# Optimization experiments

Measured on AMD Instinct MI355X. Metric: run time of the kernel, lower is better.

Reference implementation:

```python
import jax, jax.numpy as jnp
import numpy as np

N = 100000      # nodes
E = 1600000     # edges (avg degree 16)
IN_DIM = 128
H = 4           # num_heads
D = 16          # out_feats per head
EF = 32         # edge_feats
T = 8           # num_etypes
NEG_SLOPE = 0.2


def setup_inputs() -> dict:
    key = jax.random.key(0)
    ks = jax.random.split(key, 10)
    x = jax.random.normal(ks[0], (N, IN_DIM), dtype=jnp.float32)
    src = jax.random.randint(ks[1], (E,), 0, N)
    dst = jax.random.randint(ks[2], (E,), 0, N)
    etype = jax.random.randint(ks[3], (E,), 0, T)
    # learned params (xavier-ish scale)
    fc_W = jax.random.normal(ks[4], (IN_DIM, H * D), dtype=jnp.float32) * (2.0 / (IN_DIM + H * D)) ** 0.5
    fc_e_W = jax.random.normal(ks[5], (EF, H * EF), dtype=jnp.float32) * (2.0 / (EF + H * EF)) ** 0.5
    edge_emb = jax.random.normal(ks[6], (T, EF), dtype=jnp.float32)
    attn_l = jax.random.normal(ks[7], (H, D), dtype=jnp.float32) * (2.0 / (H * D)) ** 0.5
    attn_r = jax.random.normal(ks[8], (H, D), dtype=jnp.float32) * (2.0 / (H * D)) ** 0.5
    attn_e = jax.random.normal(ks[9], (H, EF), dtype=jnp.float32) * (2.0 / (H * EF)) ** 0.5
    return {"x": x, "src": src, "dst": dst, "etype": etype,
            "fc_W": fc_W, "fc_e_W": fc_e_W, "edge_emb": edge_emb,
            "attn_l": attn_l, "attn_r": attn_r, "attn_e": attn_e}


def reference(x, src, dst, etype, fc_W, fc_e_W, edge_emb, attn_l, attn_r, attn_e):
    n = x.shape[0]
    # node projection: [N, H, D]
    feat = (x @ fc_W).reshape(n, H, D)
    el = jnp.einsum('nhd,hd->nh', feat, attn_l)   # [N, H]
    er = jnp.einsum('nhd,hd->nh', feat, attn_r)   # [N, H]
    # per-etype edge scalar: edge_emb @ fc_e -> [T, H, EF] -> [T, H]
    ef = (edge_emb @ fc_e_W).reshape(T, H, EF)
    ee = jnp.einsum('the,he->th', ef, attn_e)
    # per-edge attention logits, leaky relu  [E, H]
    s = jax.nn.leaky_relu(el[src] + er[dst] + ee[etype], NEG_SLOPE)
    # edge_softmax over incoming edges of each dst (homogeneous graph)
    smax = jax.ops.segment_max(s, dst, num_segments=n)
    p = jnp.exp(s - smax[dst])
    denom = jax.ops.segment_sum(p, dst, num_segments=n)
    a = p / denom[dst]                             # [E, H]
    # gather-mul-scatter aggregation: sum_e a_e * feat[src_e]
    msg = feat[src] * a[:, :, None]                # [E, H, D]
    rst = jax.ops.segment_sum(msg, dst, num_segments=n)  # [N, H, D]
    return rst
```

## Files before the change

kernel.cpp:

```cpp
#include <hip/hip_runtime.h>

#define NH 4
#define HD 64
#define IN_DIM 128
#define NEG_SLOPE 0.2f
#define BN 64
#define NBMAX 1664
#define SLAB 2048
#define CHUNK 4096
#define EPT (CHUNK/512)
#define SBUFSZ 2048
#define NGEMM 256

typedef short bf8 __attribute__((ext_vector_type(8)));
typedef float f4  __attribute__((ext_vector_type(4)));

__device__ inline unsigned short f2bf(float f) {
  unsigned u = __float_as_uint(f);
  u += 0x7FFFu + ((u >> 16) & 1u);
  return (unsigned short)(u >> 16);
}

__global__ __launch_bounds__(512) void k_combo(
    const float* __restrict__ x, const float* __restrict__ fcW,
    const float* __restrict__ attn_l, const float* __restrict__ attn_r,
    unsigned short* __restrict__ featb, float4* __restrict__ el4, float4* __restrict__ er4,
    const int* __restrict__ src, const int* __restrict__ dst, const int* __restrict__ et,
    int* __restrict__ cntg, unsigned* __restrict__ ebuf,
    const float* __restrict__ edge_emb, const float* __restrict__ fc_e_W,
    const float* __restrict__ attn_e, float* __restrict__ ee,
    int n, int ne, int nb, int ngemm, int nchunks)
{
  __shared__ union {
    struct {
      int scnt[NBMAX];
      unsigned short sbase[NBMAX];
      unsigned short goff[NBMAX];
      unsigned sbuf[CHUNK];
      int wsm[8], wbs[8];
    } m;
    unsigned short wt[HD][IN_DIM + 8];
    float sef[8][128];
  } sm;

  const int t = threadIdx.x;
  const int lane = t & 63, wv = t >> 6;

  if (blockIdx.x < ngemm) {
    for (int idx = t; idx < IN_DIM * HD; idx += 512) {
      int k = idx >> 6, j = idx & 63;
      sm.wt[j][k] = f2bf(fcW[idx]);
    }
    __syncthreads();

    const int lr = lane & 15;
    const int lg = lane >> 4;
    float al[NH], ar[NH];
#pragma unroll
    for (int h = 0; h < NH; ++h) { al[h] = attn_l[h * 16 + lr]; ar[h] = attn_r[h * 16 + lr]; }

    const int ntp = (n + 127) >> 7;
    for (int tp = blockIdx.x; tp < ntp; tp += ngemm) {
      const int rowbase = tp * 128 + wv * 16;
      int arow = rowbase + lr;
      if (arow >= n) arow = n - 1;
      const float* xp = x + (size_t)arow * IN_DIM + lg * 8;

      f4 acc[4] = {};
#pragma unroll
      for (int kc = 0; kc < 4; ++kc) {
        float4 a0 = *(const float4*)(xp + kc * 32);
        float4 a1 = *(const float4*)(xp + kc * 32 + 4);
        bf8 af;
        af[0] = (short)f2bf(a0.x); af[1] = (short)f2bf(a0.y);
        af[2] = (short)f2bf(a0.z); af[3] = (short)f2bf(a0.w);
        af[4] = (short)f2bf(a1.x); af[5] = (short)f2bf(a1.y);
        af[6] = (short)f2bf(a1.z); af[7] = (short)f2bf(a1.w);
#pragma unroll
        for (int nt = 0; nt < 4; ++nt) {
          bf8 bfr = *(const bf8*)&sm.wt[nt * 16 + lr][kc * 32 + lg * 8];
          acc[nt] = __builtin_amdgcn_mfma_f32_16x16x32_bf16(af, bfr, acc[nt], 0, 0, 0);
        }
      }

#pragma unroll
      for (int r = 0; r < 4; ++r) {
        int grow = rowbase + lg * 4 + r;
        bool ok = grow < n;
        if (ok) {
#pragma unroll
          for (int nt = 0; nt < 4; ++nt)
            featb[(size_t)grow * HD + nt * 16 + lr] = f2bf(acc[nt][r]);
        }
        float pl[NH], pr[NH];
#pragma unroll
        for (int h = 0; h < NH; ++h) { pl[h] = acc[h][r] * al[h]; pr[h] = acc[h][r] * ar[h]; }
#pragma unroll
        for (int off = 1; off < 16; off <<= 1) {
#pragma unroll
          for (int h = 0; h < NH; ++h) {
            pl[h] += __shfl_xor(pl[h], off);
            pr[h] += __shfl_xor(pr[h], off);
          }
        }
        if (ok && lr == 0) {
          el4[grow] = make_float4(pl[0], pl[1], pl[2], pl[3]);
          er4[grow] = make_float4(pr[0], pr[1], pr[2], pr[3]);
        }
      }
    }
    return;
  }

  if (blockIdx.x >= ngemm + nchunks) {
    if (t < 128) {
      for (int r = 0; r < 8; ++r) {
        float acc = 0.f;
#pragma unroll
        for (int k = 0; k < 32; ++k) acc = fmaf(edge_emb[r * 32 + k], fc_e_W[k * 128 + t], acc);
        sm.sef[r][t] = acc;
      }
    }
    __syncthreads();
    if (t < 32) {
      int r = t >> 2, h = t & 3;
      float acc = 0.f;
#pragma unroll
      for (int e2 = 0; e2 < 32; ++e2) acc += sm.sef[r][h * 32 + e2] * attn_e[h * 32 + e2];
      ee[r * NH + h] = acc;
    }
    return;
  }

  const int base = (blockIdx.x - ngemm) * CHUNK;
  for (int i = t; i < nb; i += 512) sm.m.scnt[i] = 0;
  __syncthreads();
  unsigned pk[EPT], rc[EPT];
#pragma unroll
  for (int i = 0; i < EPT; ++i) {
    int e = base + i * 512 + t;
    pk[i] = 0xFFFFFFFFu;
    if (e < ne) {
      int d = dst[e];
      int bin = d >> 6;
      rc[i] = (unsigned)src[e] | ((unsigned)et[e] << 17) | ((unsigned)(d & 63) << 20);
      int slot = atomicAdd(&sm.m.scnt[bin], 1);
      pk[i] = ((unsigned)slot << 11) | (unsigned)bin;
    }
  }
  __syncthreads();
  int c[4], s = 0;
#pragma unroll
  for (int j = 0; j < 4; ++j) { int b = 4 * t + j; c[j] = (b < nb) ? sm.m.scnt[b] : 0; s += c[j]; }
  int inc = s;
#pragma unroll
  for (int off = 1; off < 64; off <<= 1) {
    int v = __shfl_up(inc, off);
    if (lane >= off) inc += v;
  }
  if (lane == 63) sm.m.wsm[wv] = inc;
  __syncthreads();
  if (t == 0) { int r = 0; for (int k = 0; k < 8; ++k) { sm.m.wbs[k] = r; r += sm.m.wsm[k]; } }
  __syncthreads();
  int ex = sm.m.wbs[wv] + inc - s;
#pragma unroll
  for (int j = 0; j < 4; ++j) {
    int b = 4 * t + j;
    if (b < nb) {
      sm.m.sbase[b] = (unsigned short)ex;
      if (c[j] > 0) {
        int raw = atomicAdd(&cntg[b], c[j]);
        sm.m.goff[b] = (unsigned short)(raw < SLAB ? raw : SLAB);
      }
    }
    ex += c[j];
  }
  __syncthreads();
#pragma unroll
  for (int i = 0; i < EPT; ++i) {
    if (pk[i] != 0xFFFFFFFFu) {
      int bin = (int)(pk[i] & 2047u);
      int slot = (int)(pk[i] >> 11);
      sm.m.sbuf[(int)sm.m.sbase[bin] + slot] = rc[i];
    }
  }
  __syncthreads();
  const int sub = lane >> 3, rl = lane & 7;
  for (int b0 = wv * 8 + sub; b0 < nb; b0 += 64) {
    int cnt = sm.m.scnt[b0];
    if (cnt > 0) {
      int sb = (int)sm.m.sbase[b0];
      int go = (int)sm.m.goff[b0];
      int allowed = SLAB - go;
      if (allowed > cnt) allowed = cnt;
      unsigned* gp = ebuf + (size_t)b0 * SLAB + go;
      for (int i2 = rl; i2 < allowed; i2 += 8)
        gp[i2] = sm.m.sbuf[sb + i2];
    }
  }
}

__global__ __launch_bounds__(512) void k_sortagg(
    const unsigned* __restrict__ ebuf, const int* __restrict__ cntg,
    const float* __restrict__ el, const float4* __restrict__ er4,
    const float* __restrict__ eeg, const uint4* __restrict__ featq,
    const int* __restrict__ src, const int* __restrict__ dst, const int* __restrict__ et,
    float4* __restrict__ out4, int n, int ne)
{
  __shared__ unsigned sbuf[SBUFSZ];
  __shared__ int cnt[BN];
  __shared__ int sb[BN + 1];
  __shared__ float s_er[BN][NH];
  __shared__ float s_ee[32];
  const int t = threadIdx.x;
  const int node0 = blockIdx.x * BN;
  const int count = cntg[blockIdx.x];
  const int beg = blockIdx.x * SLAB;
  const int end = beg + count;
  for (int i = t; i < BN; i += 512) {
    cnt[i] = 0;
    int node = node0 + i;
    float4 v = (node < n) ? er4[node] : make_float4(0.f, 0.f, 0.f, 0.f);
    s_er[i][0] = v.x; s_er[i][1] = v.y; s_er[i][2] = v.z; s_er[i][3] = v.w;
  }
  if (t < 32) s_ee[t] = eeg[t];
  __syncthreads();

  const int lane = t & 63, wv = t >> 6;
  const int q = lane >> 3;
  const int l = lane & 7;
  const int h = l >> 1;
  const bool sorted = (count <= SBUFSZ);

  if (sorted) {
    unsigned rr_[SBUFSZ / 512], pk_[SBUFSZ / 512];
#pragma unroll
    for (int j = 0; j < SBUFSZ / 512; ++j) {
      int i = beg + j * 512 + t;
      pk_[j] = 0xFFFFFFFFu;
      if (i < end) {
        unsigned r = ebuf[i];
        rr_[j] = r;
        unsigned bin = r >> 20;
        unsigned slot = (unsigned)atomicAdd(&cnt[bin], 1);
        pk_[j] = (slot << 6) | bin;
      }
    }
    __syncthreads();
    if (t < 64) {
      int cc = cnt[t];
      int inc = cc;
#pragma unroll
      for (int off = 1; off < 64; off <<= 1) {
        int v = __shfl_up(inc, off);
        if (lane >= off) inc += v;
      }
      int ex = inc - cc;
      sb[t] = ex;
      if (t == 63) sb[64] = ex + cc;
    }
    __syncthreads();
#pragma unroll
    for (int j = 0; j < SBUFSZ / 512; ++j) {
      if (pk_[j] != 0xFFFFFFFFu)
        sbuf[sb[pk_[j] & 63u] + (int)(pk_[j] >> 6)] = rr_[j];
    }
    __syncthreads();
  }

  for (int ld = wv * 8; ld < wv * 8 + 8; ++ld) {
    float erh = s_er[ld][h];
    float a0 = 0.f, a1 = 0.f, a2 = 0.f, a3 = 0.f;
    float a4 = 0.f, a5 = 0.f, a6 = 0.f, a7 = 0.f, den = 0.f;
    if (sorted) {
      const int s0 = sb[ld], s1 = sb[ld + 1];
      for (int i = s0 + q; i < s1; i += 8) {
        unsigned r = sbuf[i];
        int s  = (int)(r & 0x1FFFFu);
        int tt = (int)((r >> 17) & 7u);
        float sv = el[s * NH + h] + erh + s_ee[tt * NH + h];
        sv = sv > 0.f ? sv : NEG_SLOPE * sv;
        float p = __expf(sv);
        den += p;
        uint4 u = featq[(size_t)s * 8 + l];
        a0 = fmaf(p, __uint_as_float(u.x << 16), a0);
        a1 = fmaf(p, __uint_as_float(u.x & 0xFFFF0000u), a1);
        a2 = fmaf(p, __uint_as_float(u.y << 16), a2);
        a3 = fmaf(p, __uint_as_float(u.y & 0xFFFF0000u), a3);
        a4 = fmaf(p, __uint_as_float(u.z << 16), a4);
        a5 = fmaf(p, __uint_as_float(u.z & 0xFFFF0000u), a5);
        a6 = fmaf(p, __uint_as_float(u.w << 16), a6);
        a7 = fmaf(p, __uint_as_float(u.w & 0xFFFF0000u), a7);
      }
    } else {
      int node = node0 + ld;
      for (int i = q; i < ne; i += 8) {
        if (dst[i] != node) continue;
        int s  = src[i];
        int tt = et[i];
        float sv = el[s * NH + h] + erh + s_ee[tt * NH + h];
        sv = sv > 0.f ? sv : NEG_SLOPE * sv;
        float p = __expf(sv);
        den += p;
        uint4 u = featq[(size_t)s * 8 + l];
        a0 = fmaf(p, __uint_as_float(u.x << 16), a0);
        a1 = fmaf(p, __uint_as_float(u.x & 0xFFFF0000u), a1);
        a2 = fmaf(p, __uint_as_float(u.y << 16), a2);
        a3 = fmaf(p, __uint_as_float(u.y & 0xFFFF0000u), a3);
        a4 = fmaf(p, __uint_as_float(u.z << 16), a4);
        a5 = fmaf(p, __uint_as_float(u.z & 0xFFFF0000u), a5);
        a6 = fmaf(p, __uint_as_float(u.w << 16), a6);
        a7 = fmaf(p, __uint_as_float(u.w & 0xFFFF0000u), a7);
      }
    }
#pragma unroll
    for (int off = 8; off <= 32; off <<= 1) {
      den += __shfl_xor(den, off);
      a0 += __shfl_xor(a0, off); a1 += __shfl_xor(a1, off);
      a2 += __shfl_xor(a2, off); a3 += __shfl_xor(a3, off);
      a4 += __shfl_xor(a4, off); a5 += __shfl_xor(a5, off);
      a6 += __shfl_xor(a6, off); a7 += __shfl_xor(a7, off);
    }
    if (q == 0) {
      int node = node0 + ld;
      if (node < n) {
        float inv = den > 0.f ? 1.f / den : 0.f;
        float4* op = out4 + (size_t)node * 16 + l * 2;
        op[0] = make_float4(a0 * inv, a1 * inv, a2 * inv, a3 * inv);
        op[1] = make_float4(a4 * inv, a5 * inv, a6 * inv, a7 * inv);
      }
    }
  }
}

extern "C" void kernel_launch(void* const* d_in, const int* in_sizes, int n_in,
                              void* d_out, int out_size, void* d_ws, size_t ws_size,
                              hipStream_t stream)
{
  const float* x        = (const float*)d_in[0];
  const int*   src      = (const int*)d_in[1];
  const int*   dst      = (const int*)d_in[2];
  const int*   etype    = (const int*)d_in[3];
  const float* fcW      = (const float*)d_in[4];
  const float* fceW     = (const float*)d_in[5];
  const float* edge_emb = (const float*)d_in[6];
  const float* attn_l   = (const float*)d_in[7];
  const float* attn_r   = (const float*)d_in[8];
  const float* attn_e   = (const float*)d_in[9];
  float* out = (float*)d_out;

  const int n  = in_sizes[0] / IN_DIM;
  const int ne = in_sizes[1];
  const int nb = (n + BN - 1) / BN;
  const int nchunks = (ne + CHUNK - 1) / CHUNK;

  char* ws = (char*)d_ws;
  size_t off = 0;
  unsigned short* featb = (unsigned short*)(ws + off); off += (size_t)n * HD * sizeof(unsigned short);
  float* el    = (float*)(ws + off); off += (size_t)n * NH * sizeof(float);
  float* er    = (float*)(ws + off); off += (size_t)n * NH * sizeof(float);
  float* ee    = (float*)(ws + off); off += 256;
  int* cntg    = (int*)(ws + off);   off += NBMAX * sizeof(int);
  unsigned* ebuf = (unsigned*)(ws + off); off += (size_t)NBMAX * SLAB * sizeof(unsigned);

  hipMemsetAsync(cntg, 0, NBMAX * sizeof(int), stream);

  k_combo<<<NGEMM + nchunks + 1, 512, 0, stream>>>(
      x, fcW, attn_l, attn_r, featb, (float4*)el, (float4*)er,
      src, dst, etype, cntg, ebuf, edge_emb, fceW, attn_e, ee,
      n, ne, nb, NGEMM, nchunks);
  k_sortagg<<<nb, 512, 0, stream>>>(ebuf, cntg, el, (const float4*)er, ee,
                                    (const uint4*)featb, src, dst, etype,
                                    (float4*)out, n, ne);
}
```

Measured before the change: 114.8 us.

## Widen destination bins to 256 nodes and run aggregation with 1024 threads

Each destination bin now covers 256 nodes instead of 64, with a 5120-entry slab per bin, and the aggregation kernel launches 1024-thread blocks, each wave handling 16 nodes. The bucketing kernel's per-thread bin scan is simplified to one bin per thread, and the GEMM block count is changed. The aim is fewer, larger bins: fewer global atomics on the per-bin counters, fewer blocks, and more work per block in the sort-and-aggregate pass. In exchange, each block uses more shared memory and runs a larger in-block sort, which may lower occupancy, and some bins can overflow the slab and fall back to the unsorted path.

Result: faster. 104.8 us (-8.7%).

```diff
diff --git a/kernel.cpp b/kernel.cpp
--- a/kernel.cpp
+++ b/kernel.cpp
@@ -4,13 +4,13 @@
 #define HD 64
 #define IN_DIM 128
 #define NEG_SLOPE 0.2f
-#define BN 64
-#define NBMAX 1664
-#define SLAB 2048
+#define BN 256
+#define NBMAX 512
+#define SLAB 5120
 #define CHUNK 4096
 #define EPT (CHUNK/512)
-#define SBUFSZ 2048
-#define NGEMM 256
+#define SBUFSZ SLAB
+#define NGEMM 391
 
 typedef short bf8 __attribute__((ext_vector_type(8)));
 typedef float f4  __attribute__((ext_vector_type(4)));
@@ -142,17 +142,15 @@
     pk[i] = 0xFFFFFFFFu;
     if (e < ne) {
       int d = dst[e];
-      int bin = d >> 6;
-      rc[i] = (unsigned)src[e] | ((unsigned)et[e] << 17) | ((unsigned)(d & 63) << 20);
+      int bin = d >> 8;
+      rc[i] = (unsigned)src[e] | ((unsigned)et[e] << 17) | ((unsigned)(d & 255) << 20);
       int slot = atomicAdd(&sm.m.scnt[bin], 1);
-      pk[i] = ((unsigned)slot << 11) | (unsigned)bin;
-    }
-  }
-  __syncthreads();
-  int c[4], s = 0;
-#pragma unroll
-  for (int j = 0; j < 4; ++j) { int b = 4 * t + j; c[j] = (b < nb) ? sm.m.scnt[b] : 0; s += c[j]; }
-  int inc = s;
+      pk[i] = ((unsigned)slot << 9) | (unsigned)bin;
+    }
+  }
+  __syncthreads();
+  int c = (t < nb) ? sm.m.scnt[t] : 0;
+  int inc = c;
 #pragma unroll
   for (int off = 1; off < 64; off <<= 1) {
     int v = __shfl_up(inc, off);
@@ -162,25 +160,20 @@
   __syncthreads();
   if (t == 0) { int r = 0; for (int k = 0; k < 8; ++k) { sm.m.wbs[k] = r; r += sm.m.wsm[k]; } }
   __syncthreads();
-  int ex = sm.m.wbs[wv] + inc - s;
-#pragma unroll
-  for (int j = 0; j < 4; ++j) {
-    int b = 4 * t + j;
-    if (b < nb) {
-      sm.m.sbase[b] = (unsigned short)ex;
-      if (c[j] > 0) {
-        int raw = atomicAdd(&cntg[b], c[j]);
-        sm.m.goff[b] = (unsigned short)(raw < SLAB ? raw : SLAB);
-      }
-    }
-    ex += c[j];
+  int ex = sm.m.wbs[wv] + inc - c;
+  if (t < nb) {
+    sm.m.sbase[t] = (unsigned short)ex;
+    if (c > 0) {
+      int raw = atomicAdd(&cntg[t], c);
+      sm.m.goff[t] = (unsigned short)(raw < SLAB ? raw : SLAB);
+    }
   }
   __syncthreads();
 #pragma unroll
   for (int i = 0; i < EPT; ++i) {
     if (pk[i] != 0xFFFFFFFFu) {
-      int bin = (int)(pk[i] & 2047u);
-      int slot = (int)(pk[i] >> 11);
+      int bin = (int)(pk[i] & 511u);
+      int slot = (int)(pk[i] >> 9);
       sm.m.sbuf[(int)sm.m.sbase[bin] + slot] = rc[i];
     }
   }
@@ -200,7 +193,7 @@
   }
 }
 
-__global__ __launch_bounds__(512) void k_sortagg(
+__global__ __launch_bounds__(1024) void k_sortagg(
     const unsigned* __restrict__ ebuf, const int* __restrict__ cntg,
     const float* __restrict__ el, const float4* __restrict__ er4,
     const float* __restrict__ eeg, const uint4* __restrict__ featq,
@@ -212,12 +205,14 @@
   __shared__ int sb[BN + 1];
   __shared__ float s_er[BN][NH];
   __shared__ float s_ee[32];
+  __shared__ int wsum[4];
   const int t = threadIdx.x;
   const int node0 = blockIdx.x * BN;
-  const int count = cntg[blockIdx.x];
+  const int count0 = cntg[blockIdx.x];
+  const int count = count0 < SLAB ? count0 : SLAB;
   const int beg = blockIdx.x * SLAB;
   const int end = beg + count;
-  for (int i = t; i < BN; i += 512) {
+  for (int i = t; i < BN; i += 1024) {
     cnt[i] = 0;
     int node = node0 + i;
     float4 v = (node < n) ? er4[node] : make_float4(0.f, 0.f, 0.f, 0.f);
@@ -230,45 +225,53 @@
   const int q = lane >> 3;
   const int l = lane & 7;
   const int h = l >> 1;
-  const bool sorted = (count <= SBUFSZ);
+  const bool sorted = (count0 <= SLAB);
 
   if (sorted) {
-    unsigned rr_[SBUFSZ / 512], pk_[SBUFSZ / 512];
-#pragma unroll
-    for (int j = 0; j < SBUFSZ / 512; ++j) {
-      int i = beg + j * 512 + t;
+    unsigned rr_[(SBUFSZ + 1023) / 1024], pk_[(SBUFSZ + 1023) / 1024];
+#pragma unroll
+    for (int j = 0; j < (SBUFSZ + 1023) / 1024; ++j) {
+      int i = beg + j * 1024 + t;
       pk_[j] = 0xFFFFFFFFu;
       if (i < end) {
         unsigned r = ebuf[i];
         rr_[j] = r;
         unsigned bin = r >> 20;
         unsigned slot = (unsigned)atomicAdd(&cnt[bin], 1);
-        pk_[j] = (slot << 6) | bin;
-      }
-    }
-    __syncthreads();
-    if (t < 64) {
-      int cc = cnt[t];
-      int inc = cc;
+        pk_[j] = (slot << 8) | bin;
+      }
+    }
+    __syncthreads();
+    int cc = 0, inc = 0;
+    if (t < BN) {
+      cc = cnt[t];
+      inc = cc;
 #pragma unroll
       for (int off = 1; off < 64; off <<= 1) {
         int v = __shfl_up(inc, off);
         if (lane >= off) inc += v;
       }
-      int ex = inc - cc;
+      if (lane == 63) wsum[wv] = inc;
+    }
+    __syncthreads();
+    if (t < BN) {
+      int base = 0;
+#pragma unroll
+      for (int k = 0; k < 4; ++k) if (k < wv) base += wsum[k];
+      int ex = base + inc - cc;
       sb[t] = ex;
-      if (t == 63) sb[64] = ex + cc;
-    }
-    __syncthreads();
-#pragma unroll
-    for (int j = 0; j < SBUFSZ / 512; ++j) {
+      if (t == BN - 1) sb[BN] = ex + cc;
+    }
+    __syncthreads();
+#pragma unroll
+    for (int j = 0; j < (SBUFSZ + 1023) / 1024; ++j) {
       if (pk_[j] != 0xFFFFFFFFu)
-        sbuf[sb[pk_[j] & 63u] + (int)(pk_[j] >> 6)] = rr_[j];
-    }
-    __syncthreads();
-  }
-
-  for (int ld = wv * 8; ld < wv * 8 + 8; ++ld) {
+        sbuf[sb[pk_[j] & 255u] + (int)(pk_[j] >> 8)] = rr_[j];
+    }
+    __syncthreads();
+  }
+
+  for (int ld = wv * 16; ld < wv * 16 + 16; ++ld) {
     float erh = s_er[ld][h];
     float a0 = 0.f, a1 = 0.f, a2 = 0.f, a3 = 0.f;
     float a4 = 0.f, a5 = 0.f, a6 = 0.f, a7 = 0.f, den = 0.f;
@@ -369,7 +372,7 @@
       x, fcW, attn_l, attn_r, featb, (float4*)el, (float4*)er,
       src, dst, etype, cntg, ebuf, edge_emb, fceW, attn_e, ee,
       n, ne, nb, NGEMM, nchunks);
-  k_sortagg<<<nb, 512, 0, stream>>>(ebuf, cntg, el, (const float4*)er, ee,
-                                    (const uint4*)featb, src, dst, etype,
-                                    (float4*)out, n, ne);
+  k_sortagg<<<nb, 1024, 0, stream>>>(ebuf, cntg, el, (const float4*)er, ee,
+                                     (const uint4*)featb, src, dst, etype,
+                                     (float4*)out, n, ne);
 }
```
